# Kernel tuning notes

Measured on AMD Instinct MI355X. Metric: run time of the kernel, lower is better.

The kernel has to match this reference:

```python
import jax, jax.numpy as jnp
import numpy as np

N, D = 4096, 512
TAU, ALPHA, EPS = 0.2, 0.5, 1e-15
L2_EPS = 1e-12  # F.normalize eps


def setup_inputs() -> dict:
    key = jax.random.key(0)
    ks = jax.random.split(key, 12)
    # xavier_normal_ with gain=1.414 for [D, D] linears
    std = 1.414 * (2.0 / (D + D)) ** 0.5
    xn = lambda k: jax.random.normal(k, (D, D), jnp.float32) * std
    return {
        "z1": jax.random.normal(ks[0], (N, D), jnp.float32),
        "z2": jax.random.normal(ks[1], (N, D), jnp.float32),
        # local projector: Linear -> PReLU -> Linear
        "lw1": xn(ks[2]), "lb1": jnp.zeros((D,), jnp.float32),
        "la": jnp.full((1,), 0.25, jnp.float32),  # PReLU weight (torch default 0.25)
        "lw2": xn(ks[3]), "lb2": jnp.zeros((D,), jnp.float32),
        # global projector
        "gw1": xn(ks[4]), "gb1": jnp.zeros((D,), jnp.float32),
        "ga": jnp.full((1,), 0.25, jnp.float32),
        "gw2": xn(ks[5]), "gb2": jnp.zeros((D,), jnp.float32),
        # discriminator bilinear weight
        "W": xn(ks[6]),
        # binary positive-pair mask [N, N]
        "mask": jax.random.randint(ks[7], (N, N), 0, 2, jnp.int32),
    }


def _prelu(x, a):
    return jnp.where(x >= 0, x, a * x)


def _proj(z, w1, b1, a, w2, b2):
    # nn.Sequential(Linear, PReLU, Linear); torch Linear: z @ W.T + b
    return _prelu(z @ w1.T + b1, a[0]) @ w2.T + b2


def _l2norm(z):
    n = jnp.linalg.norm(z, axis=-1, keepdims=True)
    return z / jnp.maximum(n, L2_EPS)


def _infonce(h1, h2, m, tau):
    a = _l2norm(h1)
    b = _l2norm(h2)
    sim_intra = jnp.exp(a @ a.T / tau)  # [N, N]
    sim_inter = jnp.exp(a @ b.T / tau)  # [N, N]
    num = (sim_inter * m).sum(1)
    den = sim_intra.sum(1) + sim_inter.sum(1) - (sim_intra * m).sum(1)
    return (-jnp.log(num / den)).mean()


def reference(z1, z2, lw1, lb1, la, lw2, lb2, gw1, gb1, ga, gw2, gb2, W, mask):
    m = mask.astype(jnp.float32)
    # local (node-level) InfoNCE through the local projector
    h1 = _proj(z1, lw1, lb1, la, lw2, lb2)
    h2 = _proj(z2, lw1, lb1, la, lw2, lb2)
    local = 0.5 * (_infonce(h1, h2, m, TAU) + _infonce(h2, h1, m.T, TAU))

    # global (DGI-style) loss
    def gloss(pos_z, neg_z):
        s = pos_z.mean(0)                               # readout [D]
        h = _proj(s, gw1, gb1, ga, gw2, gb2)            # global projector [D]
        summ = W @ h                                    # [D]
        d_pos = jax.nn.sigmoid(pos_z @ summ)            # [N]
        d_neg = jax.nn.sigmoid(neg_z @ summ)            # [N]
        pos_loss = -jnp.log(d_pos + EPS).mean()
        neg_loss = -jnp.log(1.0 - d_neg + EPS).mean()
        return 0.5 * (pos_loss + neg_loss)

    glob = 0.5 * (gloss(z1, z2) + gloss(z2, z1))
    return ALPHA * local + (1.0 - ALPHA) * glob
```

## Files before the change

### kernel.cpp

```cpp
#include <hip/hip_runtime.h>
#include <math.h>

#define NN 4096
#define DD 512
#define INV_TAU 5.0f
#define EPSV 1e-15f

typedef unsigned short u16;
typedef __attribute__((ext_vector_type(8))) short short8;
typedef __attribute__((ext_vector_type(4))) float f32x4;

__device__ __forceinline__ void gld16(const void* g, void* l) {
  __builtin_amdgcn_global_load_lds(
      (const __attribute__((address_space(1))) unsigned int*)g,
      (__attribute__((address_space(3))) unsigned int*)l, 16, 0, 0);
}

__device__ __forceinline__ void bar_vm4() {
  asm volatile("s_waitcnt vmcnt(4) lgkmcnt(0)\n\ts_barrier" ::: "memory");
}
__device__ __forceinline__ void bar_vm2() {
  asm volatile("s_waitcnt vmcnt(2) lgkmcnt(0)\n\ts_barrier" ::: "memory");
}
__device__ __forceinline__ void bar_vm1() {
  asm volatile("s_waitcnt vmcnt(1) lgkmcnt(0)\n\ts_barrier" ::: "memory");
}
__device__ __forceinline__ void bar_vm0() {
  asm volatile("s_waitcnt vmcnt(0) lgkmcnt(0)\n\ts_barrier" ::: "memory");
}

__device__ __forceinline__ float bf2f(u16 u) {
  return __uint_as_float(((unsigned)u) << 16);
}
__device__ __forceinline__ u16 f2bf(float x) {
  unsigned u = __float_as_uint(x);
  u += 0x7fff + ((u >> 16) & 1);
  return (u16)(u >> 16);
}

__device__ __forceinline__ float wave_sum(float v) {
#pragma unroll
  for (int o = 32; o > 0; o >>= 1) v += __shfl_down(v, o, 64);
  return v;
}

__global__ __launch_bounds__(256) void tobf16cm(
    const float* __restrict__ a, const float* __restrict__ b,
    const float* __restrict__ c, const float* __restrict__ d2,
    u16* __restrict__ o, float* __restrict__ pc1, float* __restrict__ pc2,
    float* __restrict__ zbf) {
  const int bid = blockIdx.x, tid = threadIdx.x;
  if (bid >= 4608) {
    const int blk = bid - 4608;
    const int r0 = blk * 32;
    float a0 = 0.f, a1 = 0.f, c0 = 0.f, c1 = 0.f;
    for (int r = r0; r < r0 + 32; ++r) {
      const size_t ro = (size_t)r * DD;
      a0 += c[ro + tid];
      a1 += c[ro + 256 + tid];
      c0 += d2[ro + tid];
      c1 += d2[ro + 256 + tid];
    }
    pc1[blk * 512 + tid] = a0;
    pc1[blk * 512 + 256 + tid] = a1;
    pc2[blk * 512 + tid] = c0;
    pc2[blk * 512 + 256 + tid] = c1;
    return;
  }
  if (bid < 128) zbf[bid * 256 + tid] = 0.f;
  const int i = bid * 256 + tid;
  int j = i;
  const float* s;
  if (j < 65536) {
    s = a + (size_t)j * 4;
  } else {
    j -= 65536;
    if (j < 65536) {
      s = b + (size_t)j * 4;
    } else {
      j -= 65536;
      if (j < 524288) {
        s = c + (size_t)j * 4;
      } else {
        j -= 524288;
        s = d2 + (size_t)j * 4;
      }
    }
  }
  float4 v = *(const float4*)s;
  unsigned long long pk = (unsigned long long)f2bf(v.x) |
                          ((unsigned long long)f2bf(v.y) << 16) |
                          ((unsigned long long)f2bf(v.z) << 32) |
                          ((unsigned long long)f2bf(v.w) << 48);
  *(unsigned long long*)&o[(size_t)i * 4] = pk;
}

template <int ACT>
__global__ __launch_bounds__(512) void gemm_mv(
    const u16* __restrict__ A, const u16* __restrict__ Bw,
    const float* __restrict__ bias, const float* __restrict__ alpha_p,
    u16* __restrict__ out, const float* __restrict__ Mw,
    const float* __restrict__ mx1, const float* __restrict__ mx2,
    const float* __restrict__ mbias, const float* __restrict__ mal,
    float* __restrict__ my1, float* __restrict__ my2) {
  __shared__ __align__(16) u16 sh[3 * 6144];
  __shared__ float svb[512];
  const int tid = threadIdx.x, w = tid >> 6, lane = tid & 63;
  if (blockIdx.x < 64) {
    const int mb = blockIdx.x;
    const int bz = mb >> 5, bx = mb & 31;
    const float* xin = bz ? mx2 : mx1;
    float* y = bz ? my2 : my1;
    if (ACT) {
      float a = 0.f;
      for (int b = 0; b < 128; ++b) a += xin[b * 512 + tid];
      svb[tid] = a * (1.f / NN);
    } else {
      svb[tid] = xin[tid];
    }
    __syncthreads();
#pragma unroll
    for (int rr = 0; rr < 2; ++rr) {
      const int row = bx * 16 + w * 2 + rr;
      float acc = 0.f;
#pragma unroll
      for (int q = 0; q < 8; ++q)
        acc = fmaf(Mw[(size_t)row * DD + lane + 64 * q], svb[lane + 64 * q],
                   acc);
      acc = wave_sum(acc);
      if (lane == 0) {
        acc += mbias[row];
        if (ACT) {
          const float al = mal[0];
          acc = (acc >= 0.f) ? acc : al * acc;
        }
        y[row] = acc;
      }
    }
    return;
  }
  const int quad = lane >> 4, m16 = lane & 15;
  const int wi = w >> 1, wj = w & 1;
  const int bid2 = blockIdx.x - 64;
  const int xcd = bid2 & 7, idx = bid2 >> 3;
  const int i0 = (4 * xcd + (idx & 3)) * 128;
  const int j0 = ((idx >> 2) & 7) * 64;
  const int bz = idx >> 5;
  const u16* Ab = A + (size_t)bz * ((size_t)NN * DD);
  u16* ob = out + (size_t)bz * ((size_t)NN * DD);
  const int roff =
      (m16 >> 1) * 64 + (((((m16 & 1) << 2) | quad) ^ (m16 >> 1)) * 8);
  const int st = (lane & 7) ^ (lane >> 3);
  const int srow = 2 * (lane >> 3) + (st >> 2);
  const int scol = (st & 3) * 8;
  const u16* gs = (w < 4) ? Ab : Bw;
  const int grow0 = ((w < 4) ? i0 + 2 * w * 16 : j0 + (w - 4) * 16) + srow;
  const int doff0 = (w < 4) ? 2 * w * 512 : 4096 + (w - 4) * 512;
  auto stage = [&](int bo, int k) {
    const int kn = k * 32;
    gld16(&gs[(size_t)grow0 * DD + kn + scol], sh + bo + doff0);
    if (w < 4)
      gld16(&gs[(size_t)(grow0 + 16) * DD + kn + scol], sh + bo + doff0 + 512);
  };
  stage(0, 0);
  stage(6144, 1);
  if (w < 4) bar_vm2(); else bar_vm1();
  f32x4 acc[2][2] = {};
  int ro = 0;
  for (int kc = 0; kc < 16; ++kc) {
    if (kc <= 13) {
      int so = ro + 12288;
      if (so >= 18432) so -= 18432;
      stage(so, kc + 2);
    }
    const u16* As = sh + ro;
    const u16* Bs = sh + ro + 4096;
    short8 ar[2], br[2];
#pragma unroll
    for (int s = 0; s < 2; ++s) {
      ar[s] = *(const short8*)&As[(wi * 32 + s * 16) * 32 + roff];
      br[s] = *(const short8*)&Bs[(wj * 32 + s * 16) * 32 + roff];
    }
    __builtin_amdgcn_s_setprio(1);
#pragma unroll
    for (int si = 0; si < 2; ++si)
#pragma unroll
      for (int sj = 0; sj < 2; ++sj)
        acc[si][sj] = __builtin_amdgcn_mfma_f32_16x16x32_bf16(
            ar[si], br[sj], acc[si][sj], 0, 0, 0);
    __builtin_amdgcn_s_setprio(0);
    if (kc <= 13) {
      if (w < 4) bar_vm2(); else bar_vm1();
    } else if (kc == 14) {
      bar_vm0();
    }
    ro += 6144;
    if (ro == 18432) ro = 0;
  }
  const float al = ACT ? alpha_p[0] : 0.f;
#pragma unroll
  for (int si = 0; si < 2; ++si)
#pragma unroll
    for (int sj = 0; sj < 2; ++sj) {
      const int col = j0 + wj * 32 + sj * 16 + m16;
      const float bv = bias[col];
#pragma unroll
      for (int r = 0; r < 4; ++r) {
        const int row = i0 + wi * 32 + si * 16 + quad * 4 + r;
        float x = acc[si][sj][r] + bv;
        if (ACT) x = (x >= 0.f) ? x : al * x;
        ob[(size_t)row * DD + col] = f2bf(x);
      }
    }
}

__global__ __launch_bounds__(256) void rownorm_mv(
    const u16* __restrict__ h, u16* __restrict__ o,
    const float* __restrict__ W, const float* __restrict__ hx1,
    const float* __restrict__ hx2, float* __restrict__ sm1,
    float* __restrict__ sm2) {
  const int bid = blockIdx.x, tid = threadIdx.x;
  const int lane = tid & 63, w = tid >> 6;
  if (bid < 256) {
    const int bz = bid >> 7, bx = bid & 127;
    const float* x = bz ? hx2 : hx1;
    float* y = bz ? sm2 : sm1;
    const int row = bx * 4 + w;
    float acc = 0.f;
#pragma unroll
    for (int q = 0; q < 8; ++q)
      acc = fmaf(W[(size_t)row * DD + lane + 64 * q], x[lane + 64 * q], acc);
    acc = wave_sum(acc);
    if (lane == 0) y[row] = acc;
    return;
  }
  const int row = (bid - 256) * 4 + w;
  const size_t base = (size_t)row * DD + lane * 8;
  short8 v = *(const short8*)&h[base];
  float f[8];
  float s = 0.f;
#pragma unroll
  for (int j = 0; j < 8; ++j) {
    f[j] = bf2f((u16)v[j]);
    s += f[j] * f[j];
  }
  s = wave_sum(s);
  const float inv = 1.f / fmaxf(sqrtf(__shfl(s, 0, 64)), 1e-12f);
  short8 r;
#pragma unroll
  for (int j = 0; j < 8; ++j) r[j] = (short)f2bf(f[j] * inv);
  *(short8*)&o[base] = r;
}

__global__ __launch_bounds__(512) void sim_mfma(
    const u16* __restrict__ na, const u16* __restrict__ nb,
    const int* __restrict__ mask, float* __restrict__ zb,
    const float* __restrict__ z1g, const float* __restrict__ z2g,
    const float* __restrict__ sm1, const float* __restrict__ sm2,
    float* __restrict__ plsP, float* __restrict__ plsN) {
  extern __shared__ __align__(16) u16 shm[];
  const int tid = threadIdx.x;
  const int w = tid >> 6, lane = tid & 63;
  if (blockIdx.y < 2) {
    const int lx = blockIdx.y * 32 + blockIdx.x;
    const int bz = lx >> 5, bx5 = lx & 31;
    const float* z = bz ? z2g : z1g;
    const float* sp = bz ? sm2 : sm1;
    const float* sn = bz ? sm1 : sm2;
    float lp = 0.f, ln_ = 0.f;
    for (int k = 0; k < 16; ++k) {
      const int row = bx5 * 128 + w * 16 + k;
      float dp = 0.f, dn = 0.f;
#pragma unroll
      for (int t = 0; t < 8; ++t) {
        const float zv = z[(size_t)row * DD + lane + 64 * t];
        dp = fmaf(zv, sp[lane + 64 * t], dp);
        dn = fmaf(zv, sn[lane + 64 * t], dn);
      }
      dp = wave_sum(dp);
      dn = wave_sum(dn);
      if (lane == 0) {
        lp += -logf(1.f / (1.f + __expf(-dp)) + EPSV);
        ln_ += -logf(1.f - 1.f / (1.f + __expf(-dn)) + EPSV);
      }
    }
    float* red = (float*)shm;
    if (lane == 0) { red[w] = lp; red[8 + w] = ln_; }
    __syncthreads();
    if (tid == 0) {
      float sP = 0.f, sN = 0.f;
      for (int q = 0; q < 8; ++q) { sP += red[q]; sN += red[8 + q]; }
      plsP[lx] = sP;
      plsN[lx] = sN;
    }
    return;
  }
  const int quad = lane >> 4, m16 = lane & 15;
  const int ig = w & 3, jh = w >> 2;
  const int i0 = (blockIdx.y - 2) * 128, j0 = blockIdx.x * 128;
  const int roff =
      (m16 >> 1) * 64 + (((((m16 & 1) << 2) | quad) ^ (m16 >> 1)) * 8);
  const int st = (lane & 7) ^ (lane >> 3);
  const int srow = 2 * (lane >> 3) + (st >> 2);
  const int scol = (st & 3) * 8;
  const int p = w >> 1, rh = (w & 1) * 64;
  const u16* gs = (p & 1) ? nb : na;
  const int gr = ((p < 2) ? i0 : j0) + rh + srow;
  u16* dst0 = shm + p * 4096 + rh * 32;
  auto stage = [&](int bo, int k) {
    const int kn = k * 32;
#pragma unroll
    for (int rr = 0; rr < 64; rr += 16)
      gld16(&gs[(size_t)(gr + rr) * DD + kn + scol], dst0 + bo + rr * 32);
  };
  stage(0, 0);
  stage(16384, 1);
  bar_vm4();
  f32x4 a11[2][4] = {}, a12[2][4] = {}, a22[2][4] = {};
  int ro = 0;
  for (int kc = 0; kc < 16; ++kc) {
    if (kc <= 13) {
      int so = ro + 32768;
      if (so >= 49152) so -= 49152;
      stage(so, kc + 2);
    }
    const u16* Ai = shm + ro;
    const u16* Bi = shm + ro + 4096;
    const u16* Aj = shm + ro + 8192;
    const u16* Bj = shm + ro + 12288;
    short8 ai0 = *(const short8*)&Ai[(ig * 32) * 32 + roff];
    short8 ai1 = *(const short8*)&Ai[(ig * 32 + 16) * 32 + roff];
    short8 bi0 = *(const short8*)&Bi[(ig * 32) * 32 + roff];
    short8 bi1 = *(const short8*)&Bi[(ig * 32 + 16) * 32 + roff];
#pragma unroll
    for (int c = 0; c < 4; ++c) {
      short8 aj = *(const short8*)&Aj[(jh * 64 + c * 16) * 32 + roff];
      short8 bj = *(const short8*)&Bj[(jh * 64 + c * 16) * 32 + roff];
      __builtin_amdgcn_s_setprio(1);
      a11[0][c] = __builtin_amdgcn_mfma_f32_16x16x32_bf16(ai0, aj, a11[0][c], 0, 0, 0);
      a11[1][c] = __builtin_amdgcn_mfma_f32_16x16x32_bf16(ai1, aj, a11[1][c], 0, 0, 0);
      a12[0][c] = __builtin_amdgcn_mfma_f32_16x16x32_bf16(ai0, bj, a12[0][c], 0, 0, 0);
      a12[1][c] = __builtin_amdgcn_mfma_f32_16x16x32_bf16(ai1, bj, a12[1][c], 0, 0, 0);
      a22[0][c] = __builtin_amdgcn_mfma_f32_16x16x32_bf16(bi0, bj, a22[0][c], 0, 0, 0);
      a22[1][c] = __builtin_amdgcn_mfma_f32_16x16x32_bf16(bi1, bj, a22[1][c], 0, 0, 0);
      __builtin_amdgcn_s_setprio(0);
    }
    if (kc <= 13) bar_vm4();
    else if (kc == 14) bar_vm0();
    ro += 16384;
    if (ro == 49152) ro = 0;
  }
  float* rred = (float*)(shm + 16384);
  float* cred = rred + 512;
  rred[tid] = 0.f;
  rred[tid + 512] = 0.f;
  __syncthreads();
  float rs11[2][4] = {}, rm11[2][4] = {}, rs12[2][4] = {}, rm12[2][4] = {};
  float cs12[4] = {}, cm12[4] = {}, cs22[4] = {}, cm22[4] = {};
#pragma unroll
  for (int t = 0; t < 2; ++t)
#pragma unroll
    for (int c = 0; c < 4; ++c) {
      const int gj = j0 + jh * 64 + c * 16 + m16;
#pragma unroll
      for (int r = 0; r < 4; ++r) {
        const int gi = i0 + ig * 32 + t * 16 + quad * 4 + r;
        const float mv = (float)mask[(size_t)gi * NN + gj];
        const float e11 = __expf(a11[t][c][r] * INV_TAU);
        const float e12 = __expf(a12[t][c][r] * INV_TAU);
        const float e22 = __expf(a22[t][c][r] * INV_TAU);
        rs11[t][r] += e11;
        rm11[t][r] += e11 * mv;
        rs12[t][r] += e12;
        rm12[t][r] += e12 * mv;
        cs12[c] += e12;
        cm12[c] += e12 * mv;
        cs22[c] += e22;
        cm22[c] += e22 * mv;
      }
    }
#pragma unroll
  for (int t = 0; t < 2; ++t)
#pragma unroll
    for (int r = 0; r < 4; ++r) {
      float v0 = rs11[t][r], v1 = rm11[t][r], v2 = rs12[t][r], v3 = rm12[t][r];
#pragma unroll
      for (int o = 1; o < 16; o <<= 1) {
        v0 += __shfl_xor(v0, o, 64);
        v1 += __shfl_xor(v1, o, 64);
        v2 += __shfl_xor(v2, o, 64);
        v3 += __shfl_xor(v3, o, 64);
      }
      if (m16 == 0) {
        const int il = ig * 32 + t * 16 + quad * 4 + r;
        atomicAdd(&rred[0 * 128 + il], v0);
        atomicAdd(&rred[1 * 128 + il], v1);
        atomicAdd(&rred[2 * 128 + il], v2);
        atomicAdd(&rred[3 * 128 + il], v3);
      }
    }
#pragma unroll
  for (int c = 0; c < 4; ++c) {
    float v0 = cs12[c], v1 = cm12[c], v2 = cs22[c], v3 = cm22[c];
    v0 += __shfl_xor(v0, 16, 64); v0 += __shfl_xor(v0, 32, 64);
    v1 += __shfl_xor(v1, 16, 64); v1 += __shfl_xor(v1, 32, 64);
    v2 += __shfl_xor(v2, 16, 64); v2 += __shfl_xor(v2, 32, 64);
    v3 += __shfl_xor(v3, 16, 64); v3 += __shfl_xor(v3, 32, 64);
    if (lane < 16) {
      const int jl = jh * 64 + c * 16 + lane;
      atomicAdd(&cred[0 * 128 + jl], v0);
      atomicAdd(&cred[1 * 128 + jl], v1);
      atomicAdd(&cred[2 * 128 + jl], v2);
      atomicAdd(&cred[3 * 128 + jl], v3);
    }
  }
  __syncthreads();
  if (tid < 128) {
#pragma unroll
    for (int q = 0; q < 4; ++q)
      atomicAdd(&zb[q * NN + i0 + tid], rred[q * 128 + tid]);
  } else if (tid < 256) {
    const int jl = tid - 128;
#pragma unroll
    for (int q = 0; q < 4; ++q)
      atomicAdd(&zb[(4 + q) * NN + j0 + jl], cred[q * 128 + jl]);
  }
}

__global__ __launch_bounds__(512) void fin(const float* __restrict__ zb,
                                           const float* __restrict__ plsP,
                                           const float* __restrict__ plsN,
                                           float* __restrict__ out) {
  const int tid = threadIdx.x;
  const int lane = tid & 63, w = tid >> 6;
  float S1 = 0.f, S2 = 0.f;
#pragma unroll
  for (int k = 0; k < 8; ++k) {
    const int i = tid + k * 512;
    const float r11 = zb[i], r11m = zb[NN + i];
    const float r12 = zb[2 * NN + i], r12m = zb[3 * NN + i];
    const float c12 = zb[4 * NN + i], c12m = zb[5 * NN + i];
    const float c22 = zb[6 * NN + i], c22m = zb[7 * NN + i];
    S1 += -logf(r12m / (r11 + r12 - r11m));
    S2 += -logf(c12m / (c22 + c12 - c22m));
  }
  float G = (tid < 64) ? (plsP[tid] + plsN[tid]) : 0.f;
  S1 = wave_sum(S1);
  S2 = wave_sum(S2);
  G = wave_sum(G);
  __shared__ float fr[3][8];
  if (lane == 0) { fr[0][w] = S1; fr[1][w] = S2; fr[2][w] = G; }
  __syncthreads();
  if (tid == 0) {
    float s1t = 0.f, s2t = 0.f, gt = 0.f;
    for (int q = 0; q < 8; ++q) {
      s1t += fr[0][q];
      s2t += fr[1][q];
      gt += fr[2][q];
    }
    const float local = 0.5f * (s1t + s2t) * (1.f / NN);
    const float glob = 0.25f * gt * (1.f / NN);
    out[0] = 0.5f * local + 0.5f * glob;
  }
}

extern "C" void kernel_launch(void* const* d_in, const int* in_sizes, int n_in,
                              void* d_out, int out_size, void* d_ws,
                              size_t ws_size, hipStream_t stream) {
  const float* z1 = (const float*)d_in[0];
  const float* z2 = (const float*)d_in[1];
  const float* lw1 = (const float*)d_in[2];
  const float* lb1 = (const float*)d_in[3];
  const float* la = (const float*)d_in[4];
  const float* lw2 = (const float*)d_in[5];
  const float* lb2 = (const float*)d_in[6];
  const float* gw1 = (const float*)d_in[7];
  const float* gb1 = (const float*)d_in[8];
  const float* ga = (const float*)d_in[9];
  const float* gw2 = (const float*)d_in[10];
  const float* gb2 = (const float*)d_in[11];
  const float* W = (const float*)d_in[12];
  const int* mask = (const int*)d_in[13];
  float* out = (float*)d_out;

  static bool attr_set = false;
  if (!attr_set) {
    (void)hipFuncSetAttribute(reinterpret_cast<const void*>(sim_mfma),
                              hipFuncAttributeMaxDynamicSharedMemorySize,
                              98304);
    attr_set = true;
  }

  const size_t ND = (size_t)NN * DD;
  u16* W1b = (u16*)d_ws;
  u16* W2b = W1b + 512 * 512;
  u16* Ab = W1b + 2 * 512 * 512;
  u16* Bb = Ab + 2 * ND;
  float* zbf = (float*)(Bb + 2 * ND);
  float* pc1 = zbf + 8 * NN;
  float* pc2 = pc1 + 128 * 512;
  float* t1 = pc2 + 128 * 512;
  float* t2 = t1 + 512;
  float* hg1 = t2 + 512;
  float* hg2 = hg1 + 512;
  float* summ1 = hg2 + 512;
  float* summ2 = summ1 + 512;
  float* plsP = summ2 + 512;
  float* plsN = plsP + 64;

  tobf16cm<<<4736, dim3(256), 0, stream>>>(lw1, lw2, z1, z2, W1b, pc1, pc2,
                                           zbf);
  gemm_mv<1><<<576, dim3(512), 0, stream>>>(Ab, W1b, lb1, la, Bb, gw1, pc1,
                                            pc2, gb1, ga, t1, t2);
  gemm_mv<0><<<576, dim3(512), 0, stream>>>(Bb, W2b, lb2, la, Ab, gw2, t1, t2,
                                            gb2, nullptr, hg1, hg2);
  rownorm_mv<<<2304, dim3(256), 0, stream>>>(Ab, Bb, W, hg1, hg2, summ1,
                                             summ2);
  sim_mfma<<<dim3(32, 34), dim3(512), 98304, stream>>>(
      Bb, Bb + ND, mask, zbf, z1, z2, summ1, summ2, plsP, plsN);
  fin<<<1, dim3(512), 0, stream>>>(zbf, plsP, plsN, out);
}
```

Baseline: 257.2 us.

## Use double-buffered static LDS in sim kernel to raise occupancy and batch mask loads

```diff
diff --git a/kernel.cpp b/kernel.cpp
--- a/kernel.cpp
+++ b/kernel.cpp
@@ -7,6 +7,7 @@
 #define EPSV 1e-15f
 
 typedef unsigned short u16;
+typedef unsigned long long u64;
 typedef __attribute__((ext_vector_type(8))) short short8;
 typedef __attribute__((ext_vector_type(4))) float f32x4;
 
@@ -16,9 +17,6 @@
       (__attribute__((address_space(3))) unsigned int*)l, 16, 0, 0);
 }
 
-__device__ __forceinline__ void bar_vm4() {
-  asm volatile("s_waitcnt vmcnt(4) lgkmcnt(0)\n\ts_barrier" ::: "memory");
-}
 __device__ __forceinline__ void bar_vm2() {
   asm volatile("s_waitcnt vmcnt(2) lgkmcnt(0)\n\ts_barrier" ::: "memory");
 }
@@ -88,11 +86,9 @@
     }
   }
   float4 v = *(const float4*)s;
-  unsigned long long pk = (unsigned long long)f2bf(v.x) |
-                          ((unsigned long long)f2bf(v.y) << 16) |
-                          ((unsigned long long)f2bf(v.z) << 32) |
-                          ((unsigned long long)f2bf(v.w) << 48);
-  *(unsigned long long*)&o[(size_t)i * 4] = pk;
+  u64 pk = (u64)f2bf(v.x) | ((u64)f2bf(v.y) << 16) | ((u64)f2bf(v.z) << 32) |
+           ((u64)f2bf(v.w) << 48);
+  *(u64*)&o[(size_t)i * 4] = pk;
 }
 
 template <int ACT>
@@ -252,13 +248,13 @@
   *(short8*)&o[base] = r;
 }
 
-__global__ __launch_bounds__(512) void sim_mfma(
+__global__ __launch_bounds__(512, 4) void sim_mfma(
     const u16* __restrict__ na, const u16* __restrict__ nb,
     const int* __restrict__ mask, float* __restrict__ zb,
     const float* __restrict__ z1g, const float* __restrict__ z2g,
     const float* __restrict__ sm1, const float* __restrict__ sm2,
     float* __restrict__ plsP, float* __restrict__ plsN) {
-  extern __shared__ __align__(16) u16 shm[];
+  __shared__ __align__(16) u16 shm[2 * 4 * 4096];
   const int tid = threadIdx.x;
   const int w = tid >> 6, lane = tid & 63;
   if (blockIdx.y < 2) {
@@ -314,16 +310,11 @@
       gld16(&gs[(size_t)(gr + rr) * DD + kn + scol], dst0 + bo + rr * 32);
   };
   stage(0, 0);
-  stage(16384, 1);
-  bar_vm4();
+  bar_vm0();
   f32x4 a11[2][4] = {}, a12[2][4] = {}, a22[2][4] = {};
   int ro = 0;
   for (int kc = 0; kc < 16; ++kc) {
-    if (kc <= 13) {
-      int so = ro + 32768;
-      if (so >= 49152) so -= 49152;
-      stage(so, kc + 2);
-    }
+    if (kc < 15) stage(ro ^ 16384, kc + 1);
     const u16* Ai = shm + ro;
     const u16* Bi = shm + ro + 4096;
     const u16* Aj = shm + ro + 8192;
@@ -345,12 +336,12 @@
       a22[1][c] = __builtin_amdgcn_mfma_f32_16x16x32_bf16(bi1, bj, a22[1][c], 0, 0, 0);
       __builtin_amdgcn_s_setprio(0);
     }
-    if (kc <= 13) bar_vm4();
-    else if (kc == 14) bar_vm0();
-    ro += 16384;
-    if (ro == 49152) ro = 0;
-  }
-  float* rred = (float*)(shm + 16384);
+    if (kc < 15) {
+      bar_vm0();
+      ro ^= 16384;
+    }
+  }
+  float* rred = (float*)shm;
   float* cred = rred + 512;
   rred[tid] = 0.f;
   rred[tid + 512] = 0.f;
@@ -358,14 +349,20 @@
   float rs11[2][4] = {}, rm11[2][4] = {}, rs12[2][4] = {}, rm12[2][4] = {};
   float cs12[4] = {}, cm12[4] = {}, cs22[4] = {}, cm22[4] = {};
 #pragma unroll
-  for (int t = 0; t < 2; ++t)
+  for (int t = 0; t < 2; ++t) {
+    int mreg[4][4];
+#pragma unroll
+    for (int r = 0; r < 4; ++r) {
+      const int gi = i0 + ig * 32 + t * 16 + quad * 4 + r;
+      const int* mrow = &mask[(size_t)gi * NN + j0 + jh * 64];
+#pragma unroll
+      for (int c = 0; c < 4; ++c) mreg[r][c] = mrow[c * 16 + m16];
+    }
 #pragma unroll
     for (int c = 0; c < 4; ++c) {
-      const int gj = j0 + jh * 64 + c * 16 + m16;
 #pragma unroll
       for (int r = 0; r < 4; ++r) {
-        const int gi = i0 + ig * 32 + t * 16 + quad * 4 + r;
-        const float mv = (float)mask[(size_t)gi * NN + gj];
+        const float mv = (float)mreg[r][c];
         const float e11 = __expf(a11[t][c][r] * INV_TAU);
         const float e12 = __expf(a12[t][c][r] * INV_TAU);
         const float e22 = __expf(a22[t][c][r] * INV_TAU);
@@ -379,6 +376,7 @@
         cm22[c] += e22 * mv;
       }
     }
+  }
 #pragma unroll
   for (int t = 0; t < 2; ++t)
 #pragma unroll
@@ -483,14 +481,6 @@
   const int* mask = (const int*)d_in[13];
   float* out = (float*)d_out;
 
-  static bool attr_set = false;
-  if (!attr_set) {
-    (void)hipFuncSetAttribute(reinterpret_cast<const void*>(sim_mfma),
-                              hipFuncAttributeMaxDynamicSharedMemorySize,
-                              98304);
-    attr_set = true;
-  }
-
   const size_t ND = (size_t)NN * DD;
   u16* W1b = (u16*)d_ws;
   u16* W2b = W1b + 512 * 512;
@@ -516,7 +506,7 @@
                                             gb2, nullptr, hg1, hg2);
   rownorm_mv<<<2304, dim3(256), 0, stream>>>(Ab, Bb, W, hg1, hg2, summ1,
                                              summ2);
-  sim_mfma<<<dim3(32, 34), dim3(512), 98304, stream>>>(
+  sim_mfma<<<dim3(32, 34), dim3(512), 0, stream>>>(
       Bb, Bb + ND, mask, zbf, z1, z2, summ1, summ2, plsP, plsN);
   fin<<<1, dim3(512), 0, stream>>>(zbf, plsP, plsN, out);
 }
```

After: 288.6 us. 1.12x slower.

## Fuse projector MLP, z conversion, column sums and row-normalize into one kernel

Applied to the files above, without the earlier changes.

```diff
diff --git a/kernel.cpp b/kernel.cpp
--- a/kernel.cpp
+++ b/kernel.cpp
@@ -7,6 +7,7 @@
 #define EPSV 1e-15f
 
 typedef unsigned short u16;
+typedef unsigned long long u64;
 typedef __attribute__((ext_vector_type(8))) short short8;
 typedef __attribute__((ext_vector_type(4))) float f32x4;
 
@@ -19,12 +20,6 @@
 __device__ __forceinline__ void bar_vm4() {
   asm volatile("s_waitcnt vmcnt(4) lgkmcnt(0)\n\ts_barrier" ::: "memory");
 }
-__device__ __forceinline__ void bar_vm2() {
-  asm volatile("s_waitcnt vmcnt(2) lgkmcnt(0)\n\ts_barrier" ::: "memory");
-}
-__device__ __forceinline__ void bar_vm1() {
-  asm volatile("s_waitcnt vmcnt(1) lgkmcnt(0)\n\ts_barrier" ::: "memory");
-}
 __device__ __forceinline__ void bar_vm0() {
   asm volatile("s_waitcnt vmcnt(0) lgkmcnt(0)\n\ts_barrier" ::: "memory");
 }
@@ -44,219 +39,243 @@
   return v;
 }
 
-__global__ __launch_bounds__(256) void tobf16cm(
-    const float* __restrict__ a, const float* __restrict__ b,
-    const float* __restrict__ c, const float* __restrict__ d2,
-    u16* __restrict__ o, float* __restrict__ pc1, float* __restrict__ pc2,
-    float* __restrict__ zbf) {
+__global__ __launch_bounds__(256) void tobf16w(const float* __restrict__ a,
+                                               const float* __restrict__ b,
+                                               u16* __restrict__ o,
+                                               float* __restrict__ zbf) {
   const int bid = blockIdx.x, tid = threadIdx.x;
-  if (bid >= 4608) {
-    const int blk = bid - 4608;
-    const int r0 = blk * 32;
-    float a0 = 0.f, a1 = 0.f, c0 = 0.f, c1 = 0.f;
-    for (int r = r0; r < r0 + 32; ++r) {
-      const size_t ro = (size_t)r * DD;
-      a0 += c[ro + tid];
-      a1 += c[ro + 256 + tid];
-      c0 += d2[ro + tid];
-      c1 += d2[ro + 256 + tid];
-    }
-    pc1[blk * 512 + tid] = a0;
-    pc1[blk * 512 + 256 + tid] = a1;
-    pc2[blk * 512 + tid] = c0;
-    pc2[blk * 512 + 256 + tid] = c1;
-    return;
-  }
   if (bid < 128) zbf[bid * 256 + tid] = 0.f;
   const int i = bid * 256 + tid;
-  int j = i;
-  const float* s;
-  if (j < 65536) {
-    s = a + (size_t)j * 4;
-  } else {
-    j -= 65536;
-    if (j < 65536) {
-      s = b + (size_t)j * 4;
-    } else {
-      j -= 65536;
-      if (j < 524288) {
-        s = c + (size_t)j * 4;
-      } else {
-        j -= 524288;
-        s = d2 + (size_t)j * 4;
-      }
-    }
-  }
+  const float* s = (i < 65536) ? a + (size_t)i * 4 : b + (size_t)(i - 65536) * 4;
   float4 v = *(const float4*)s;
-  unsigned long long pk = (unsigned long long)f2bf(v.x) |
-                          ((unsigned long long)f2bf(v.y) << 16) |
-                          ((unsigned long long)f2bf(v.z) << 32) |
-                          ((unsigned long long)f2bf(v.w) << 48);
-  *(unsigned long long*)&o[(size_t)i * 4] = pk;
-}
-
-template <int ACT>
-__global__ __launch_bounds__(512) void gemm_mv(
-    const u16* __restrict__ A, const u16* __restrict__ Bw,
-    const float* __restrict__ bias, const float* __restrict__ alpha_p,
-    u16* __restrict__ out, const float* __restrict__ Mw,
-    const float* __restrict__ mx1, const float* __restrict__ mx2,
-    const float* __restrict__ mbias, const float* __restrict__ mal,
-    float* __restrict__ my1, float* __restrict__ my2) {
-  __shared__ __align__(16) u16 sh[3 * 6144];
-  __shared__ float svb[512];
+  u64 pk = (u64)f2bf(v.x) | ((u64)f2bf(v.y) << 16) | ((u64)f2bf(v.z) << 32) |
+           ((u64)f2bf(v.w) << 48);
+  *(u64*)&o[(size_t)i * 4] = pk;
+}
+
+__global__ __launch_bounds__(512) void head_fused(
+    const float* __restrict__ z1, const float* __restrict__ z2,
+    const u16* __restrict__ W1b, const u16* __restrict__ W2b,
+    const float* __restrict__ lb1, const float* __restrict__ la,
+    const float* __restrict__ lb2, u16* __restrict__ NAb,
+    float* __restrict__ pc1, float* __restrict__ pc2) {
+  extern __shared__ __align__(16) u16 shm[];
+  u16* Atile = shm;
+  u16* Wb0 = shm + 16384;
+  u16* Wb1 = shm + 32768;
   const int tid = threadIdx.x, w = tid >> 6, lane = tid & 63;
-  if (blockIdx.x < 64) {
-    const int mb = blockIdx.x;
-    const int bz = mb >> 5, bx = mb & 31;
-    const float* xin = bz ? mx2 : mx1;
-    float* y = bz ? my2 : my1;
-    if (ACT) {
-      float a = 0.f;
-      for (int b = 0; b < 128; ++b) a += xin[b * 512 + tid];
-      svb[tid] = a * (1.f / NN);
-    } else {
-      svb[tid] = xin[tid];
-    }
-    __syncthreads();
-#pragma unroll
-    for (int rr = 0; rr < 2; ++rr) {
-      const int row = bx * 16 + w * 2 + rr;
-      float acc = 0.f;
-#pragma unroll
-      for (int q = 0; q < 8; ++q)
-        acc = fmaf(Mw[(size_t)row * DD + lane + 64 * q], svb[lane + 64 * q],
-                   acc);
-      acc = wave_sum(acc);
-      if (lane == 0) {
-        acc += mbias[row];
-        if (ACT) {
-          const float al = mal[0];
-          acc = (acc >= 0.f) ? acc : al * acc;
-        }
-        y[row] = acc;
-      }
-    }
-    return;
-  }
   const int quad = lane >> 4, m16 = lane & 15;
-  const int wi = w >> 1, wj = w & 1;
-  const int bid2 = blockIdx.x - 64;
-  const int xcd = bid2 & 7, idx = bid2 >> 3;
-  const int i0 = (4 * xcd + (idx & 3)) * 128;
-  const int j0 = ((idx >> 2) & 7) * 64;
-  const int bz = idx >> 5;
-  const u16* Ab = A + (size_t)bz * ((size_t)NN * DD);
-  u16* ob = out + (size_t)bz * ((size_t)NN * DD);
+  const int bid = blockIdx.x;
+  const int bz = bid >> 7, band = bid & 127;
+  const int i0 = band * 32;
+  const float* zsrc = bz ? z2 : z1;
+  u16* ob = NAb + (size_t)bz * ((size_t)NN * DD);
+  float* pcd = bz ? pc2 : pc1;
   const int roff =
       (m16 >> 1) * 64 + (((((m16 & 1) << 2) | quad) ^ (m16 >> 1)) * 8);
   const int st = (lane & 7) ^ (lane >> 3);
   const int srow = 2 * (lane >> 3) + (st >> 2);
   const int scol = (st & 3) * 8;
-  const u16* gs = (w < 4) ? Ab : Bw;
-  const int grow0 = ((w < 4) ? i0 + 2 * w * 16 : j0 + (w - 4) * 16) + srow;
-  const int doff0 = (w < 4) ? 2 * w * 512 : 4096 + (w - 4) * 512;
-  auto stage = [&](int bo, int k) {
+  auto stageW = [&](const u16* Wsrc, int k, u16* dst) {
     const int kn = k * 32;
-    gld16(&gs[(size_t)grow0 * DD + kn + scol], sh + bo + doff0);
-    if (w < 4)
-      gld16(&gs[(size_t)(grow0 + 16) * DD + kn + scol], sh + bo + doff0 + 512);
+#pragma unroll
+    for (int rr = 0; rr < 64; rr += 16)
+      gld16(&Wsrc[(size_t)(w * 64 + rr + srow) * DD + kn + scol],
+            dst + (w * 64 + rr) * 32);
   };
-  stage(0, 0);
-  stage(6144, 1);
-  if (w < 4) bar_vm2(); else bar_vm1();
-  f32x4 acc[2][2] = {};
-  int ro = 0;
+  stageW(W1b, 0, Wb0);
+  float* pcs = (float*)(shm + 32768);
+  {
+    const int sub = tid >> 7;
+    const int c0 = (tid & 127) * 4;
+    const int c = c0 >> 5, cc = c0 & 31;
+    const int eg = (cc >> 3) & 3, inner = cc & 7;
+    float p0 = 0.f, p1 = 0.f, p2 = 0.f, p3 = 0.f;
+#pragma unroll
+    for (int rr = 0; rr < 8; ++rr) {
+      const int row = rr * 4 + sub;
+      float4 v = *(const float4*)&zsrc[(size_t)(i0 + row) * DD + c0];
+      p0 += v.x; p1 += v.y; p2 += v.z; p3 += v.w;
+      u64 pk = (u64)f2bf(v.x) | ((u64)f2bf(v.y) << 16) |
+               ((u64)f2bf(v.z) << 32) | ((u64)f2bf(v.w) << 48);
+      const int g = row >> 4, r15 = row & 15, p = r15 >> 1, rl = r15 & 1;
+      const int l = p * 8 + ((rl * 4 + eg) ^ p);
+      *(u64*)&Atile[c * 1024 + g * 512 + l * 8 + inner] = pk;
+    }
+    *(float4*)&pcs[sub * 512 + c0] = make_float4(p0, p1, p2, p3);
+  }
+  __syncthreads();
+  {
+    float s4 = pcs[tid] + pcs[512 + tid] + pcs[1024 + tid] + pcs[1536 + tid];
+    pcd[band * 512 + tid] = s4;
+  }
+  bar_vm0();
+  f32x4 acc[2][4] = {};
   for (int kc = 0; kc < 16; ++kc) {
-    if (kc <= 13) {
-      int so = ro + 12288;
-      if (so >= 18432) so -= 18432;
-      stage(so, kc + 2);
-    }
-    const u16* As = sh + ro;
-    const u16* Bs = sh + ro + 4096;
-    short8 ar[2], br[2];
-#pragma unroll
-    for (int s = 0; s < 2; ++s) {
-      ar[s] = *(const short8*)&As[(wi * 32 + s * 16) * 32 + roff];
-      br[s] = *(const short8*)&Bs[(wj * 32 + s * 16) * 32 + roff];
-    }
+    if (kc < 15) stageW(W1b, kc + 1, (kc & 1) ? Wb0 : Wb1);
+    const u16* Wc = (kc & 1) ? Wb1 : Wb0;
+    short8 ar[2], br[4];
+    ar[0] = *(const short8*)&Atile[kc * 1024 + roff];
+    ar[1] = *(const short8*)&Atile[kc * 1024 + 512 + roff];
+#pragma unroll
+    for (int sj = 0; sj < 4; ++sj)
+      br[sj] = *(const short8*)&Wc[(w * 64 + sj * 16) * 32 + roff];
     __builtin_amdgcn_s_setprio(1);
 #pragma unroll
     for (int si = 0; si < 2; ++si)
 #pragma unroll
-      for (int sj = 0; sj < 2; ++sj)
+      for (int sj = 0; sj < 4; ++sj)
         acc[si][sj] = __builtin_amdgcn_mfma_f32_16x16x32_bf16(
             ar[si], br[sj], acc[si][sj], 0, 0, 0);
     __builtin_amdgcn_s_setprio(0);
-    if (kc <= 13) {
-      if (w < 4) bar_vm2(); else bar_vm1();
-    } else if (kc == 14) {
-      bar_vm0();
-    }
-    ro += 6144;
-    if (ro == 18432) ro = 0;
-  }
-  const float al = ACT ? alpha_p[0] : 0.f;
+    if (kc < 15) bar_vm0();
+  }
+  __syncthreads();
+  stageW(W2b, 0, Wb0);
+  {
+    const float al = la[0];
+#pragma unroll
+    for (int si = 0; si < 2; ++si)
+#pragma unroll
+      for (int sj = 0; sj < 4; ++sj) {
+        const int col = w * 64 + sj * 16 + m16;
+        const float bv = lb1[col];
+        const int c = col >> 5, cc = col & 31;
+        const int eg = (cc >> 3) & 3, inner = cc & 7;
+#pragma unroll
+        for (int r = 0; r < 4; ++r) {
+          const int r15 = quad * 4 + r;
+          const int p = r15 >> 1, rl = r15 & 1;
+          const int l = p * 8 + ((rl * 4 + eg) ^ p);
+          float x = acc[si][sj][r] + bv;
+          x = (x >= 0.f) ? x : al * x;
+          Atile[c * 1024 + si * 512 + l * 8 + inner] = f2bf(x);
+        }
+      }
+  }
+  bar_vm0();
+  f32x4 a2[2][4] = {};
+  for (int kc = 0; kc < 16; ++kc) {
+    if (kc < 15) stageW(W2b, kc + 1, (kc & 1) ? Wb0 : Wb1);
+    const u16* Wc = (kc & 1) ? Wb1 : Wb0;
+    short8 ar[2], br[4];
+    ar[0] = *(const short8*)&Atile[kc * 1024 + roff];
+    ar[1] = *(const short8*)&Atile[kc * 1024 + 512 + roff];
+#pragma unroll
+    for (int sj = 0; sj < 4; ++sj)
+      br[sj] = *(const short8*)&Wc[(w * 64 + sj * 16) * 32 + roff];
+    __builtin_amdgcn_s_setprio(1);
+#pragma unroll
+    for (int si = 0; si < 2; ++si)
+#pragma unroll
+      for (int sj = 0; sj < 4; ++sj)
+        a2[si][sj] = __builtin_amdgcn_mfma_f32_16x16x32_bf16(
+            ar[si], br[sj], a2[si][sj], 0, 0, 0);
+    __builtin_amdgcn_s_setprio(0);
+    if (kc < 15) bar_vm0();
+  }
+  __syncthreads();
+  float* ns = (float*)(shm + 16384);
+  float fl[2][4][4];
+  float ssr[2][4] = {};
 #pragma unroll
   for (int si = 0; si < 2; ++si)
 #pragma unroll
-    for (int sj = 0; sj < 2; ++sj) {
-      const int col = j0 + wj * 32 + sj * 16 + m16;
-      const float bv = bias[col];
+    for (int sj = 0; sj < 4; ++sj) {
+      const float bv = lb2[w * 64 + sj * 16 + m16];
 #pragma unroll
       for (int r = 0; r < 4; ++r) {
-        const int row = i0 + wi * 32 + si * 16 + quad * 4 + r;
-        float x = acc[si][sj][r] + bv;
-        if (ACT) x = (x >= 0.f) ? x : al * x;
-        ob[(size_t)row * DD + col] = f2bf(x);
-      }
-    }
-}
-
-__global__ __launch_bounds__(256) void rownorm_mv(
-    const u16* __restrict__ h, u16* __restrict__ o,
-    const float* __restrict__ W, const float* __restrict__ hx1,
-    const float* __restrict__ hx2, float* __restrict__ sm1,
-    float* __restrict__ sm2) {
+        const float f = bf2f(f2bf(a2[si][sj][r] + bv));
+        fl[si][sj][r] = f;
+        ssr[si][r] = fmaf(f, f, ssr[si][r]);
+      }
+    }
+#pragma unroll
+  for (int si = 0; si < 2; ++si)
+#pragma unroll
+    for (int r = 0; r < 4; ++r) {
+      float v = ssr[si][r];
+      v += __shfl_xor(v, 1, 64);
+      v += __shfl_xor(v, 2, 64);
+      v += __shfl_xor(v, 4, 64);
+      v += __shfl_xor(v, 8, 64);
+      if (m16 == 0) ns[(si * 16 + quad * 4 + r) * 8 + w] = v;
+    }
+  __syncthreads();
+  if (tid < 32) {
+    float s = 0.f;
+#pragma unroll
+    for (int q = 0; q < 8; ++q) s += ns[tid * 8 + q];
+    ns[256 + tid] = 1.f / fmaxf(sqrtf(s), 1e-12f);
+  }
+  __syncthreads();
+#pragma unroll
+  for (int si = 0; si < 2; ++si)
+#pragma unroll
+    for (int r = 0; r < 4; ++r) {
+      const int row = si * 16 + quad * 4 + r;
+      const float inv = ns[256 + row];
+#pragma unroll
+      for (int sj = 0; sj < 4; ++sj) {
+        const int col = w * 64 + sj * 16 + m16;
+        ob[(size_t)(i0 + row) * DD + col] = f2bf(fl[si][sj][r] * inv);
+      }
+    }
+}
+
+__global__ __launch_bounds__(256) void mvh(
+    const float* __restrict__ pc1, const float* __restrict__ pc2,
+    const float* __restrict__ gw1, const float* __restrict__ gb1,
+    const float* __restrict__ ga, const float* __restrict__ gw2,
+    const float* __restrict__ gb2, float* __restrict__ hg) {
+  __shared__ float svb[512], tvb[512];
   const int bid = blockIdx.x, tid = threadIdx.x;
+  const int bz = bid >> 6, sub = bid & 63;
+  const float* pc = bz ? pc2 : pc1;
   const int lane = tid & 63, w = tid >> 6;
-  if (bid < 256) {
-    const int bz = bid >> 7, bx = bid & 127;
-    const float* x = bz ? hx2 : hx1;
-    float* y = bz ? sm2 : sm1;
-    const int row = bx * 4 + w;
+  {
+    float a0 = 0.f, a1 = 0.f;
+    for (int b = 0; b < 128; ++b) {
+      a0 += pc[b * 512 + tid];
+      a1 += pc[b * 512 + 256 + tid];
+    }
+    svb[tid] = a0 * (1.f / NN);
+    svb[256 + tid] = a1 * (1.f / NN);
+  }
+  __syncthreads();
+  const float al = ga[0];
+  for (int rr = 0; rr < 128; ++rr) {
+    const int row = w * 128 + rr;
     float acc = 0.f;
 #pragma unroll
     for (int q = 0; q < 8; ++q)
-      acc = fmaf(W[(size_t)row * DD + lane + 64 * q], x[lane + 64 * q], acc);
+      acc = fmaf(gw1[(size_t)row * DD + lane + 64 * q], svb[lane + 64 * q],
+                 acc);
     acc = wave_sum(acc);
-    if (lane == 0) y[row] = acc;
-    return;
-  }
-  const int row = (bid - 256) * 4 + w;
-  const size_t base = (size_t)row * DD + lane * 8;
-  short8 v = *(const short8*)&h[base];
-  float f[8];
-  float s = 0.f;
-#pragma unroll
-  for (int j = 0; j < 8; ++j) {
-    f[j] = bf2f((u16)v[j]);
-    s += f[j] * f[j];
-  }
-  s = wave_sum(s);
-  const float inv = 1.f / fmaxf(sqrtf(__shfl(s, 0, 64)), 1e-12f);
-  short8 r;
-#pragma unroll
-  for (int j = 0; j < 8; ++j) r[j] = (short)f2bf(f[j] * inv);
-  *(short8*)&o[base] = r;
+    if (lane == 0) {
+      acc += gb1[row];
+      tvb[row] = (acc >= 0.f) ? acc : al * acc;
+    }
+  }
+  __syncthreads();
+#pragma unroll
+  for (int rr = 0; rr < 2; ++rr) {
+    const int row = sub * 8 + w * 2 + rr;
+    float acc = 0.f;
+#pragma unroll
+    for (int q = 0; q < 8; ++q)
+      acc = fmaf(gw2[(size_t)row * DD + lane + 64 * q], tvb[lane + 64 * q],
+                 acc);
+    acc = wave_sum(acc);
+    if (lane == 0) hg[bz * 512 + row] = acc + gb2[row];
+  }
 }
 
 __global__ __launch_bounds__(512) void sim_mfma(
     const u16* __restrict__ na, const u16* __restrict__ nb,
     const int* __restrict__ mask, float* __restrict__ zb,
     const float* __restrict__ z1g, const float* __restrict__ z2g,
-    const float* __restrict__ sm1, const float* __restrict__ sm2,
+    const float* __restrict__ Wd, const float* __restrict__ hg,
     float* __restrict__ plsP, float* __restrict__ plsN) {
   extern __shared__ __align__(16) u16 shm[];
   const int tid = threadIdx.x;
@@ -264,9 +283,26 @@
   if (blockIdx.y < 2) {
     const int lx = blockIdx.y * 32 + blockIdx.x;
     const int bz = lx >> 5, bx5 = lx & 31;
+    float* smP = (float*)shm;
+    float* smN = smP + 512;
+    float* red = smN + 512;
+#pragma unroll
+    for (int q = 0; q < 2; ++q) {
+      const float* hgq = hg + q * 512;
+      float* dst = (q == bz) ? smP : smN;
+      for (int rr = 0; rr < 64; ++rr) {
+        const int row = w * 64 + rr;
+        float acc = 0.f;
+#pragma unroll
+        for (int t = 0; t < 8; ++t)
+          acc = fmaf(Wd[(size_t)row * DD + lane + 64 * t], hgq[lane + 64 * t],
+                     acc);
+        acc = wave_sum(acc);
+        if (lane == 0) dst[row] = acc;
+      }
+    }
+    __syncthreads();
     const float* z = bz ? z2g : z1g;
-    const float* sp = bz ? sm2 : sm1;
-    const float* sn = bz ? sm1 : sm2;
     float lp = 0.f, ln_ = 0.f;
     for (int k = 0; k < 16; ++k) {
       const int row = bx5 * 128 + w * 16 + k;
@@ -274,8 +310,8 @@
 #pragma unroll
       for (int t = 0; t < 8; ++t) {
         const float zv = z[(size_t)row * DD + lane + 64 * t];
-        dp = fmaf(zv, sp[lane + 64 * t], dp);
-        dn = fmaf(zv, sn[lane + 64 * t], dn);
+        dp = fmaf(zv, smP[lane + 64 * t], dp);
+        dn = fmaf(zv, smN[lane + 64 * t], dn);
       }
       dp = wave_sum(dp);
       dn = wave_sum(dn);
@@ -284,7 +320,6 @@
         ln_ += -logf(1.f - 1.f / (1.f + __expf(-dn)) + EPSV);
       }
     }
-    float* red = (float*)shm;
     if (lane == 0) { red[w] = lp; red[8 + w] = ln_; }
     __syncthreads();
     if (tid == 0) {
@@ -488,35 +523,27 @@
     (void)hipFuncSetAttribute(reinterpret_cast<const void*>(sim_mfma),
                               hipFuncAttributeMaxDynamicSharedMemorySize,
                               98304);
+    (void)hipFuncSetAttribute(reinterpret_cast<const void*>(head_fused),
+                              hipFuncAttributeMaxDynamicSharedMemorySize,
+                              98304);
     attr_set = true;
   }
 
   const size_t ND = (size_t)NN * DD;
   u16* W1b = (u16*)d_ws;
-  u16* W2b = W1b + 512 * 512;
-  u16* Ab = W1b + 2 * 512 * 512;
-  u16* Bb = Ab + 2 * ND;
-  float* zbf = (float*)(Bb + 2 * ND);
+  u16* NAb = W1b + 2 * 512 * 512;
+  float* zbf = (float*)(NAb + 2 * ND);
   float* pc1 = zbf + 8 * NN;
   float* pc2 = pc1 + 128 * 512;
-  float* t1 = pc2 + 128 * 512;
-  float* t2 = t1 + 512;
-  float* hg1 = t2 + 512;
-  float* hg2 = hg1 + 512;
-  float* summ1 = hg2 + 512;
-  float* summ2 = summ1 + 512;
-  float* plsP = summ2 + 512;
+  float* hg = pc2 + 128 * 512;
+  float* plsP = hg + 1024;
   float* plsN = plsP + 64;
 
-  tobf16cm<<<4736, dim3(256), 0, stream>>>(lw1, lw2, z1, z2, W1b, pc1, pc2,
-                                           zbf);
-  gemm_mv<1><<<576, dim3(512), 0, stream>>>(Ab, W1b, lb1, la, Bb, gw1, pc1,
-                                            pc2, gb1, ga, t1, t2);
-  gemm_mv<0><<<576, dim3(512), 0, stream>>>(Bb, W2b, lb2, la, Ab, gw2, t1, t2,
-                                            gb2, nullptr, hg1, hg2);
-  rownorm_mv<<<2304, dim3(256), 0, stream>>>(Ab, Bb, W, hg1, hg2, summ1,
-                                             summ2);
+  tobf16w<<<512, dim3(256), 0, stream>>>(lw1, lw2, W1b, zbf);
+  head_fused<<<256, dim3(512), 98304, stream>>>(
+      z1, z2, W1b, W1b + 512 * 512, lb1, la, lb2, NAb, pc1, pc2);
+  mvh<<<128, dim3(256), 0, stream>>>(pc1, pc2, gw1, gb1, ga, gw2, gb2, hg);
   sim_mfma<<<dim3(32, 34), dim3(512), 98304, stream>>>(
-      Bb, Bb + ND, mask, zbf, z1, z2, summ1, summ2, plsP, plsN);
+      NAb, NAb + ND, mask, zbf, z1, z2, W, hg, plsP, plsN);
   fin<<<1, dim3(512), 0, stream>>>(zbf, plsP, plsN, out);
 }
```

Measured after the change: 337.7 us. +31.3%, slower.
